# Performance work log

Measured on AMD Instinct MI355X. Metric: run time of the kernel, lower is better.

The kernel has to match this reference:

```python
import jax, jax.numpy as jnp
import numpy as np

B, S, H = 4, 2048, 1024   # batch, seq_len, hidden_dim
E, D = 8, 1024            # num_experts, expert_dim (== hidden per module structure)
TOP_K = 2


def setup_inputs() -> dict:
    key = jax.random.key(0)
    ks = jax.random.split(key, 8)
    scale_h = 1.0 / np.sqrt(H)
    scale_d = 1.0 / np.sqrt(D)
    return {
        "x": jax.random.normal(ks[0], (B, S, H), dtype=jnp.float32),
        # router linear: hidden -> num_experts
        "w_router": jax.random.normal(ks[1], (H, E), dtype=jnp.float32) * scale_h,
        "b_router": jnp.zeros((E,), dtype=jnp.float32),
        # per-expert linear: hidden -> expert_dim
        "w_experts": jax.random.normal(ks[2], (E, H, D), dtype=jnp.float32) * scale_h,
        "b_experts": jnp.zeros((E, D), dtype=jnp.float32),
        # output linear: expert_dim -> expert_dim
        "w_out": jax.random.normal(ks[3], (D, D), dtype=jnp.float32) * scale_d,
        "b_out": jnp.zeros((D,), dtype=jnp.float32),
    }


def reference(x, w_router, b_router, w_experts, b_experts, w_out, b_out):
    # --- MoERouter: softmax over expert logits, top-2, renormalize ---
    logits = jnp.einsum("bsh,he->bse", x, w_router) + b_router          # [B,S,E]
    probs = jax.nn.softmax(logits, axis=-1)
    top_p, top_i = jax.lax.top_k(probs, TOP_K)                           # [B,S,2]
    top_p = top_p / jnp.sum(top_p, axis=-1, keepdims=True)
    # --- Dense expert compute over all tokens (module computes every expert) ---
    expert_out = jnp.einsum("bsh,ehd->bsed", x, w_experts) + b_experts   # [B,S,E,D]
    expert_out = jax.nn.gelu(expert_out)
    # --- Gather top-2 expert outputs and combine with routing weights ---
    sel = jnp.take_along_axis(expert_out, top_i[..., None], axis=2)      # [B,S,2,D]
    combined = jnp.sum(sel * top_p[..., None], axis=2)                   # [B,S,D]
    # --- Output projection ---
    return jnp.einsum("bsd,de->bse", combined, w_out) + b_out
```

## Files before the change

kernel.cpp:

```cpp
#include <hip/hip_runtime.h>


#define TOKENS 8192
#define HDIM   1024
#define DDIM   1024
#define NEXP   8

typedef __bf16 bf16x8 __attribute__((ext_vector_type(8)));
typedef float  f32x4  __attribute__((ext_vector_type(4)));

__device__ __forceinline__ unsigned short f2b(float f) {
  unsigned int u = __builtin_bit_cast(unsigned int, f);
  u = u + 0x7fffu + ((u >> 16) & 1u);
  return (unsigned short)(u >> 16);
}
__device__ __forceinline__ float b2f(unsigned short b) {
  unsigned int u = ((unsigned int)b) << 16;
  return __builtin_bit_cast(float, u);
}

__device__ __forceinline__ void gld_lds16(const void* g, void* l) {
  __builtin_amdgcn_global_load_lds(
      (__attribute__((address_space(1))) void*)(g),
      (__attribute__((address_space(3))) void*)(l),
      16, 0, 0);
}


__global__ __launch_bounds__(256) void pre_kernel(
    const float* __restrict__ x, const float* __restrict__ wr,
    const float* __restrict__ br,
    const float* __restrict__ we, const float* __restrict__ wo,
    unsigned short* __restrict__ weT, unsigned short* __restrict__ woT,
    unsigned short* __restrict__ xb,
    int* __restrict__ eidx, float* __restrict__ ew) {
  __shared__ unsigned short tile[32][33];
  int tid = threadIdx.x;
  if (blockIdx.x >= 2048) {
    int lid = blockIdx.x - 2048;
    int z = lid >> 10;
    int rem = lid & 1023;
    int bx = (rem & 31) * 32;
    int by = (rem >> 5) * 32;
    const float* s;
    unsigned short* d;
    if (z < 8) { s = we + (size_t)z * HDIM * DDIM; d = weT + (size_t)z * HDIM * DDIM; }
    else       { s = wo;                            d = woT; }
    int tx = tid & 31, ty = tid >> 5;
    for (int i = ty; i < 32; i += 8)
      tile[i][tx] = f2b(s[(size_t)(by + i) * 1024 + bx + tx]);
    __syncthreads();
    for (int i = ty; i < 32; i += 8)
      d[(size_t)(bx + i) * 1024 + by + tx] = tile[tx][i];
    return;
  }
  int wave = tid >> 6, lane = tid & 63;
  int t = blockIdx.x * 4 + wave;
  const float* xp = x + (size_t)t * HDIM;
  unsigned short* xbp = xb + (size_t)t * HDIM;
  float acc[8];
#pragma unroll
  for (int e = 0; e < 8; ++e) acc[e] = 0.f;
#pragma unroll
  for (int h0 = 0; h0 < HDIM; h0 += 256) {
    int h = h0 + lane * 4;
    float4 xv = *(const float4*)&xp[h];
    ushort4 o;
    o.x = f2b(xv.x); o.y = f2b(xv.y); o.z = f2b(xv.z); o.w = f2b(xv.w);
    *(ushort4*)&xbp[h] = o;
    float xq[4] = {xv.x, xv.y, xv.z, xv.w};
#pragma unroll
    for (int q = 0; q < 4; ++q) {
      const float4* wp = (const float4*)&wr[(h + q) * 8];
      float4 w0 = wp[0], w1 = wp[1];
      acc[0] += xq[q] * w0.x; acc[1] += xq[q] * w0.y; acc[2] += xq[q] * w0.z; acc[3] += xq[q] * w0.w;
      acc[4] += xq[q] * w1.x; acc[5] += xq[q] * w1.y; acc[6] += xq[q] * w1.z; acc[7] += xq[q] * w1.w;
    }
  }
#pragma unroll
  for (int off = 32; off; off >>= 1)
#pragma unroll
    for (int e = 0; e < 8; ++e) acc[e] += __shfl_xor(acc[e], off, 64);
  if (lane == 0) {
    float l[8], p[8];
    float m = -1e30f;
#pragma unroll
    for (int e = 0; e < 8; ++e) { l[e] = acc[e] + br[e]; m = fmaxf(m, l[e]); }
    float s = 0.f;
#pragma unroll
    for (int e = 0; e < 8; ++e) { p[e] = __expf(l[e] - m); s += p[e]; }
    int i1 = 0;
#pragma unroll
    for (int e = 1; e < 8; ++e) if (p[e] > p[i1]) i1 = e;
    int i2 = (i1 == 0) ? 1 : 0;
#pragma unroll
    for (int e = 0; e < 8; ++e) if (e != i1 && p[e] > p[i2]) i2 = e;
    float ps = p[i1] + p[i2];
    eidx[t * 2]     = i1;  ew[t * 2]     = p[i1] / ps;
    eidx[t * 2 + 1] = i2;  ew[t * 2 + 1] = p[i2] / ps;
  }
}


__global__ __launch_bounds__(1024) void build_lists_kernel(
    const int4* __restrict__ eidx4, const float4* __restrict__ ew4,
    int* __restrict__ counts, int* __restrict__ tok2, float* __restrict__ wl) {
  int e = blockIdx.x;
  int tid = threadIdx.x;
  int lane = tid & 63, wv = tid >> 6;
  __shared__ int wsum[16];
  __shared__ int base;
  if (tid == 0) base = 0;
  __syncthreads();
#pragma unroll
  for (int c = 0; c < 4; ++c) {
    int v4 = c * 1024 + tid;
    int4   ev = eidx4[v4];
    float4 fw = ew4[v4];
    bool m0 = (ev.x == e), m1 = (ev.y == e), m2 = (ev.z == e), m3 = (ev.w == e);
    unsigned long long b0 = __ballot(m0);
    unsigned long long b1 = __ballot(m1);
    unsigned long long b2 = __ballot(m2);
    unsigned long long b3 = __ballot(m3);
    int c0 = __popcll(b0), c1 = __popcll(b1), c2 = __popcll(b2), c3 = __popcll(b3);
    if (lane == 0) wsum[wv] = c0 + c1 + c2 + c3;
    __syncthreads();
    int wbase = base;
    for (int w = 0; w < wv; ++w) wbase += wsum[w];
    unsigned long long lm = (lane == 63) ? ~0ull >> 1 : (1ull << lane) - 1ull;
    lm = (1ull << lane) - 1ull;
    int ibase = c * 4096 + tid * 4;
    int off0 = wbase;
    int off1 = off0 + c0;
    int off2 = off1 + c1;
    int off3 = off2 + c2;
    if (m0) { int p = off0 + __popcll(b0 & lm); tok2[e * TOKENS + p] = ibase + 0; wl[e * TOKENS + p] = fw.x; }
    if (m1) { int p = off1 + __popcll(b1 & lm); tok2[e * TOKENS + p] = ibase + 1; wl[e * TOKENS + p] = fw.y; }
    if (m2) { int p = off2 + __popcll(b2 & lm); tok2[e * TOKENS + p] = ibase + 2; wl[e * TOKENS + p] = fw.z; }
    if (m3) { int p = off3 + __popcll(b3 & lm); tok2[e * TOKENS + p] = ibase + 3; wl[e * TOKENS + p] = fw.w; }
    int total = 0;
#pragma unroll
    for (int w = 0; w < 16; ++w) total += wsum[w];
    __syncthreads();
    if (tid == 0) base += total;
    __syncthreads();
  }
  if (tid == 0) counts[e] = base;
}


__global__ __launch_bounds__(256, 3) void expert_gemm_kernel(
    const unsigned short* __restrict__ xb, const unsigned short* __restrict__ weT,
    const float* __restrict__ b_experts, const int* __restrict__ counts,
    const int* __restrict__ tok2, const float* __restrict__ wlist,
    unsigned short* __restrict__ outslot) {
  int b = blockIdx.x;
  int id = (b >> 3) + (b & 7) * 512;
  int e = id >> 9;
  int rem = id & 511;
  int m0 = (rem >> 3) << 7;
  int n0 = (rem & 7) << 7;
  int cnt = counts[e];
  if (m0 >= cnt) return;

  __shared__ unsigned short As[3][128 * 32];
  __shared__ unsigned short Bs[3][128 * 32];
  __shared__ int   tokS[128];
  __shared__ float wS[128];

  int tid = threadIdx.x;
  if (tid < 128) {
    int r = m0 + tid;
    tokS[tid] = (r < cnt) ? tok2[e * TOKENS + r] : 0;
    wS[tid]   = (r < cnt) ? wlist[e * TOKENS + r] : 0.f;
  }
  __syncthreads();

  int wave = tid >> 6, lane = tid & 63;
  int subr = lane >> 2, koff = (lane & 3) * 8;

  const unsigned short* wbase = weT + (size_t)e * (HDIM * DDIM);
  const unsigned short* asrc[2];
  const unsigned short* bsrc[2];
  unsigned short* adst[3][2];
  unsigned short* bdst[3][2];
#pragma unroll
  for (int i = 0; i < 2; ++i) {
    int row = i * 64 + wave * 16 + subr;
    asrc[i] = xb + (size_t)(tokS[row] >> 1) * HDIM + koff;
    bsrc[i] = wbase + (size_t)(n0 + row) * HDIM + koff;
#pragma unroll
    for (int bb = 0; bb < 3; ++bb) {
      adst[bb][i] = &As[bb][i * 2048 + wave * 512];
      bdst[bb][i] = &Bs[bb][i * 2048 + wave * 512];
    }
  }

  int wm = wave & 1, wn = wave >> 1;
  int quad = lane >> 4, lr = lane & 15;

  f32x4 zero = {0.f, 0.f, 0.f, 0.f};
  f32x4 acc[4][4];
#pragma unroll
  for (int i = 0; i < 4; ++i)
#pragma unroll
    for (int j = 0; j < 4; ++j) acc[i][j] = zero;

#pragma unroll
  for (int s = 0; s < 2; ++s)
#pragma unroll
    for (int i = 0; i < 2; ++i) {
      gld_lds16(asrc[i] + s * 32, adst[s][i]);
      gld_lds16(bsrc[i] + s * 32, bdst[s][i]);
    }

#pragma unroll
  for (int kk = 0; kk < 32; ++kk) {
    if (kk < 31) asm volatile("s_waitcnt vmcnt(4)" ::: "memory");
    else         asm volatile("s_waitcnt vmcnt(0)" ::: "memory");
    __builtin_amdgcn_s_barrier();
    if (kk + 2 < 32) {
      int nb = (kk + 2) % 3;
      int off = (kk + 2) * 32;
#pragma unroll
      for (int i = 0; i < 2; ++i) {
        gld_lds16(asrc[i] + off, adst[nb][i]);
        gld_lds16(bsrc[i] + off, bdst[nb][i]);
      }
    }
    int cb = kk % 3;
    bf16x8 af[4], bfr[4];
#pragma unroll
    for (int i = 0; i < 4; ++i)
      af[i] = *(const bf16x8*)&As[cb][(wm * 64 + i * 16 + lr) * 32 + quad * 8];
#pragma unroll
    for (int j = 0; j < 4; ++j)
      bfr[j] = *(const bf16x8*)&Bs[cb][(wn * 64 + j * 16 + lr) * 32 + quad * 8];
#pragma unroll
    for (int i = 0; i < 4; ++i)
#pragma unroll
      for (int j = 0; j < 4; ++j)
        acc[i][j] = __builtin_amdgcn_mfma_f32_16x16x32_bf16(af[i], bfr[j], acc[i][j], 0, 0, 0);
  }

#pragma unroll
  for (int j = 0; j < 4; ++j) {
    int col = n0 + wn * 64 + j * 16 + lr;
    float bias = b_experts[e * DDIM + col];
#pragma unroll
    for (int i = 0; i < 4; ++i) {
      int rbase = wm * 64 + i * 16 + quad * 4;
#pragma unroll
      for (int r = 0; r < 4; ++r) {
        int row = rbase + r;
        if (m0 + row < cnt) {
          float h = acc[i][j][r] + bias;
          float z = 0.7978845608f * (h + 0.044715f * h * h * h);
          float t = 1.f - 2.f / (__expf(2.f * z) + 1.f);
          float g = 0.5f * h * (1.f + t);
          outslot[(size_t)tokS[row] * DDIM + col] = f2b(g * wS[row]);
        }
      }
    }
  }
}


__global__ void combine_kernel(const ushort4* __restrict__ outslot, ushort4* __restrict__ comb) {
  int i = blockIdx.x * 256 + threadIdx.x;
  int t = i >> 8, d4 = i & 255;
  ushort4 a = outslot[t * 512 + d4];
  ushort4 b = outslot[t * 512 + 256 + d4];
  ushort4 o;
  o.x = f2b(b2f(a.x) + b2f(b.x));
  o.y = f2b(b2f(a.y) + b2f(b.y));
  o.z = f2b(b2f(a.z) + b2f(b.z));
  o.w = f2b(b2f(a.w) + b2f(b.w));
  comb[i] = o;
}


__global__ __launch_bounds__(256, 3) void out_gemm_kernel(
    const unsigned short* __restrict__ Abf, const unsigned short* __restrict__ BT,
    const float* __restrict__ bias, float* __restrict__ out) {
  int b = blockIdx.x;
  int id = (b >> 3) + (b & 7) * 64;
  int n0 = (id >> 6) << 7;
  int m0 = (id & 63) << 7;

  __shared__ unsigned short As[3][128 * 32];
  __shared__ unsigned short Bs[3][128 * 32];
  int tid = threadIdx.x, wave = tid >> 6, lane = tid & 63;
  int subr = lane >> 2, koff = (lane & 3) * 8;

  const unsigned short* asrc[2];
  const unsigned short* bsrc[2];
  unsigned short* adst[3][2];
  unsigned short* bdst[3][2];
#pragma unroll
  for (int i = 0; i < 2; ++i) {
    int row = i * 64 + wave * 16 + subr;
    asrc[i] = Abf + (size_t)(m0 + row) * DDIM + koff;
    bsrc[i] = BT + (size_t)(n0 + row) * DDIM + koff;
#pragma unroll
    for (int bb = 0; bb < 3; ++bb) {
      adst[bb][i] = &As[bb][i * 2048 + wave * 512];
      bdst[bb][i] = &Bs[bb][i * 2048 + wave * 512];
    }
  }

  int wm = wave & 1, wn = wave >> 1;
  int quad = lane >> 4, lr = lane & 15;

  f32x4 zero = {0.f, 0.f, 0.f, 0.f};
  f32x4 acc[4][4];
#pragma unroll
  for (int i = 0; i < 4; ++i)
#pragma unroll
    for (int j = 0; j < 4; ++j) acc[i][j] = zero;

#pragma unroll
  for (int s = 0; s < 2; ++s)
#pragma unroll
    for (int i = 0; i < 2; ++i) {
      gld_lds16(asrc[i] + s * 32, adst[s][i]);
      gld_lds16(bsrc[i] + s * 32, bdst[s][i]);
    }

#pragma unroll
  for (int kk = 0; kk < 32; ++kk) {
    if (kk < 31) asm volatile("s_waitcnt vmcnt(4)" ::: "memory");
    else         asm volatile("s_waitcnt vmcnt(0)" ::: "memory");
    __builtin_amdgcn_s_barrier();
    if (kk + 2 < 32) {
      int nb = (kk + 2) % 3;
      int off = (kk + 2) * 32;
#pragma unroll
      for (int i = 0; i < 2; ++i) {
        gld_lds16(asrc[i] + off, adst[nb][i]);
        gld_lds16(bsrc[i] + off, bdst[nb][i]);
      }
    }
    int cb = kk % 3;
    bf16x8 af[4], bfr[4];
#pragma unroll
    for (int i = 0; i < 4; ++i)
      af[i] = *(const bf16x8*)&As[cb][(wm * 64 + i * 16 + lr) * 32 + quad * 8];
#pragma unroll
    for (int j = 0; j < 4; ++j)
      bfr[j] = *(const bf16x8*)&Bs[cb][(wn * 64 + j * 16 + lr) * 32 + quad * 8];
#pragma unroll
    for (int i = 0; i < 4; ++i)
#pragma unroll
      for (int j = 0; j < 4; ++j)
        acc[i][j] = __builtin_amdgcn_mfma_f32_16x16x32_bf16(af[i], bfr[j], acc[i][j], 0, 0, 0);
  }

#pragma unroll
  for (int j = 0; j < 4; ++j) {
    int col = n0 + wn * 64 + j * 16 + lr;
    float bs = bias[col];
#pragma unroll
    for (int i = 0; i < 4; ++i) {
      int rbase = wm * 64 + i * 16 + quad * 4;
#pragma unroll
      for (int r = 0; r < 4; ++r)
        out[(size_t)(m0 + rbase + r) * DDIM + col] = acc[i][j][r] + bs;
    }
  }
}


extern "C" void kernel_launch(void* const* d_in, const int* in_sizes, int n_in,
                              void* d_out, int out_size, void* d_ws, size_t ws_size,
                              hipStream_t stream) {
  const float* x  = (const float*)d_in[0];
  const float* wr = (const float*)d_in[1];
  const float* br = (const float*)d_in[2];
  const float* we = (const float*)d_in[3];
  const float* be = (const float*)d_in[4];
  const float* wo = (const float*)d_in[5];
  const float* bo = (const float*)d_in[6];
  float* out = (float*)d_out;

  char* ws = (char*)d_ws;
  unsigned short* xb      = (unsigned short*)(ws);
  unsigned short* weT     = (unsigned short*)(ws + 16777216);
  unsigned short* woT     = (unsigned short*)(ws + 33554432);
  unsigned short* outslot = (unsigned short*)(ws + 35651584);
  int*            counts  = (int*)           (ws + 69206016);
  int*            tok2    = (int*)           (ws + 69206272);
  float*          wlist   = (float*)         (ws + 69468416);
  int*            eidx    = (int*)           (ws + 69730560);
  float*          ew      = (float*)         (ws + 69796096);
  unsigned short* comb    = xb;

  pre_kernel<<<2048 + 9216, 256, 0, stream>>>(x, wr, br, we, wo, weT, woT,
                                              xb, eidx, ew);
  build_lists_kernel<<<8, 1024, 0, stream>>>((const int4*)eidx, (const float4*)ew,
                                             counts, tok2, wlist);
  expert_gemm_kernel<<<4096, 256, 0, stream>>>(xb, weT, be, counts, tok2, wlist, outslot);
  combine_kernel<<<8192, 256, 0, stream>>>((const ushort4*)outslot, (ushort4*)comb);
  out_gemm_kernel<<<512, 256, 0, stream>>>(comb, woT, bo, out);
}
```

Baseline: 260.7 us.

## Fuse top-2 slot combine into output GEMM A-tile loading

Removes the separate combine kernel. The output GEMM now loads both expert-slot rows into registers, adds them in bf16, and writes the sum into LDS, while B tiles still use direct global-to-LDS loads. This drops one launch and the write and re-read of the combined buffer. In exchange, the A operand goes through registers with extra VALU conversion work and a changed wait/barrier schedule inside the GEMM main loop, which may reduce overlap.

Measured after the change: 271.6 us. 1.04x slower.

```diff
diff --git a/kernel.cpp b/kernel.cpp
--- a/kernel.cpp
+++ b/kernel.cpp
@@ -8,6 +8,7 @@
 
 typedef __bf16 bf16x8 __attribute__((ext_vector_type(8)));
 typedef float  f32x4  __attribute__((ext_vector_type(4)));
+typedef unsigned short u16x8 __attribute__((ext_vector_type(8)));
 
 __device__ __forceinline__ unsigned short f2b(float f) {
   unsigned int u = __builtin_bit_cast(unsigned int, f);
@@ -127,8 +128,7 @@
     __syncthreads();
     int wbase = base;
     for (int w = 0; w < wv; ++w) wbase += wsum[w];
-    unsigned long long lm = (lane == 63) ? ~0ull >> 1 : (1ull << lane) - 1ull;
-    lm = (1ull << lane) - 1ull;
+    unsigned long long lm = (1ull << lane) - 1ull;
     int ibase = c * 4096 + tid * 4;
     int off0 = wbase;
     int off1 = off0 + c0;
@@ -266,22 +266,8 @@
 }
 
 
-__global__ void combine_kernel(const ushort4* __restrict__ outslot, ushort4* __restrict__ comb) {
-  int i = blockIdx.x * 256 + threadIdx.x;
-  int t = i >> 8, d4 = i & 255;
-  ushort4 a = outslot[t * 512 + d4];
-  ushort4 b = outslot[t * 512 + 256 + d4];
-  ushort4 o;
-  o.x = f2b(b2f(a.x) + b2f(b.x));
-  o.y = f2b(b2f(a.y) + b2f(b.y));
-  o.z = f2b(b2f(a.z) + b2f(b.z));
-  o.w = f2b(b2f(a.w) + b2f(b.w));
-  comb[i] = o;
-}
-
-
 __global__ __launch_bounds__(256, 3) void out_gemm_kernel(
-    const unsigned short* __restrict__ Abf, const unsigned short* __restrict__ BT,
+    const unsigned short* __restrict__ outslot, const unsigned short* __restrict__ BT,
     const float* __restrict__ bias, float* __restrict__ out) {
   int b = blockIdx.x;
   int id = (b >> 3) + (b & 7) * 64;
@@ -293,20 +279,22 @@
   int tid = threadIdx.x, wave = tid >> 6, lane = tid & 63;
   int subr = lane >> 2, koff = (lane & 3) * 8;
 
-  const unsigned short* asrc[2];
+  const unsigned short* pa0[2];
+  const unsigned short* pa1[2];
   const unsigned short* bsrc[2];
-  unsigned short* adst[3][2];
   unsigned short* bdst[3][2];
+  int adst_off[2];
 #pragma unroll
   for (int i = 0; i < 2; ++i) {
     int row = i * 64 + wave * 16 + subr;
-    asrc[i] = Abf + (size_t)(m0 + row) * DDIM + koff;
+    int t = m0 + row;
+    pa0[i] = outslot + (size_t)t * (2 * DDIM) + koff;
+    pa1[i] = outslot + (size_t)t * (2 * DDIM) + DDIM + koff;
     bsrc[i] = BT + (size_t)(n0 + row) * DDIM + koff;
-#pragma unroll
-    for (int bb = 0; bb < 3; ++bb) {
-      adst[bb][i] = &As[bb][i * 2048 + wave * 512];
+    adst_off[i] = i * 2048 + wave * 512 + lane * 8;
+#pragma unroll
+    for (int bb = 0; bb < 3; ++bb)
       bdst[bb][i] = &Bs[bb][i * 2048 + wave * 512];
-    }
   }
 
   int wm = wave & 1, wn = wave >> 1;
@@ -319,27 +307,41 @@
 #pragma unroll
     for (int j = 0; j < 4; ++j) acc[i][j] = zero;
 
-#pragma unroll
-  for (int s = 0; s < 2; ++s)
-#pragma unroll
-    for (int i = 0; i < 2; ++i) {
-      gld_lds16(asrc[i] + s * 32, adst[s][i]);
-      gld_lds16(bsrc[i] + s * 32, bdst[s][i]);
-    }
-
-#pragma unroll
+  u16x8 ra[2], rb[2];
+#pragma unroll
+  for (int i = 0; i < 2; ++i) {
+    ra[i] = *(const u16x8*)(pa0[i]);
+    rb[i] = *(const u16x8*)(pa1[i]);
+  }
+  asm volatile("" ::: "memory");
+#pragma unroll
+  for (int i = 0; i < 2; ++i) gld_lds16(bsrc[i], bdst[0][i]);
+#pragma unroll
+  for (int i = 0; i < 2; ++i) gld_lds16(bsrc[i] + 32, bdst[1][i]);
+  asm volatile("s_waitcnt vmcnt(4)" ::: "memory");
+#pragma unroll
+  for (int i = 0; i < 2; ++i) {
+    u16x8 o;
+#pragma unroll
+    for (int q = 0; q < 8; ++q) o[q] = f2b(b2f(ra[i][q]) + b2f(rb[i][q]));
+    *(u16x8*)&As[0][adst_off[i]] = o;
+  }
+  asm volatile("s_waitcnt vmcnt(2) lgkmcnt(0)" ::: "memory");
+  __builtin_amdgcn_s_barrier();
+
   for (int kk = 0; kk < 32; ++kk) {
-    if (kk < 31) asm volatile("s_waitcnt vmcnt(4)" ::: "memory");
-    else         asm volatile("s_waitcnt vmcnt(0)" ::: "memory");
-    __builtin_amdgcn_s_barrier();
+    if (kk < 31) {
+      int off = (kk + 1) * 32;
+#pragma unroll
+      for (int i = 0; i < 2; ++i) {
+        ra[i] = *(const u16x8*)(pa0[i] + off);
+        rb[i] = *(const u16x8*)(pa1[i] + off);
+      }
+    }
     if (kk + 2 < 32) {
-      int nb = (kk + 2) % 3;
-      int off = (kk + 2) * 32;
-#pragma unroll
-      for (int i = 0; i < 2; ++i) {
-        gld_lds16(asrc[i] + off, adst[nb][i]);
-        gld_lds16(bsrc[i] + off, bdst[nb][i]);
-      }
+#pragma unroll
+      for (int i = 0; i < 2; ++i)
+        gld_lds16(bsrc[i] + (kk + 2) * 32, bdst[(kk + 2) % 3][i]);
     }
     int cb = kk % 3;
     bf16x8 af[4], bfr[4];
@@ -354,6 +356,20 @@
 #pragma unroll
       for (int j = 0; j < 4; ++j)
         acc[i][j] = __builtin_amdgcn_mfma_f32_16x16x32_bf16(af[i], bfr[j], acc[i][j], 0, 0, 0);
+    if (kk < 31) {
+      if (kk + 2 < 32) asm volatile("s_waitcnt vmcnt(2)" ::: "memory");
+      else             asm volatile("s_waitcnt vmcnt(0)" ::: "memory");
+      int nb = (kk + 1) % 3;
+#pragma unroll
+      for (int i = 0; i < 2; ++i) {
+        u16x8 o;
+#pragma unroll
+        for (int q = 0; q < 8; ++q) o[q] = f2b(b2f(ra[i][q]) + b2f(rb[i][q]));
+        *(u16x8*)&As[nb][adst_off[i]] = o;
+      }
+      asm volatile("s_waitcnt lgkmcnt(0)" ::: "memory");
+      __builtin_amdgcn_s_barrier();
+    }
   }
 
 #pragma unroll
@@ -393,13 +409,11 @@
   float*          wlist   = (float*)         (ws + 69468416);
   int*            eidx    = (int*)           (ws + 69730560);
   float*          ew      = (float*)         (ws + 69796096);
-  unsigned short* comb    = xb;
 
   pre_kernel<<<2048 + 9216, 256, 0, stream>>>(x, wr, br, we, wo, weT, woT,
                                               xb, eidx, ew);
   build_lists_kernel<<<8, 1024, 0, stream>>>((const int4*)eidx, (const float4*)ew,
                                              counts, tok2, wlist);
   expert_gemm_kernel<<<4096, 256, 0, stream>>>(xb, weT, be, counts, tok2, wlist, outslot);
-  combine_kernel<<<8192, 256, 0, stream>>>((const ushort4*)outslot, (ushort4*)comb);
-  out_gemm_kernel<<<512, 256, 0, stream>>>(comb, woT, bo, out);
-}
+  out_gemm_kernel<<<512, 256, 0, stream>>>(outslot, woT, bo, out);
+}
```
